# Kernel tuning notes

Hardware: AMD Instinct MI355X
Metric: run time of the kernel (lower is better)

## Reference

```python
import jax, jax.numpy as jnp
import numpy as np

DIM = 1024
HEADS = 16
HEAD_DIM = DIM // HEADS
SCALE = float(HEAD_DIM) ** -0.5


def setup_inputs() -> dict:
    key = jax.random.key(0)
    k1, k2, k3 = jax.random.split(key, 3)
    x = jax.random.normal(k1, (4, 2048, DIM), dtype=jnp.float32)
    w_qkv = jax.random.normal(k2, (DIM, 3 * DIM), dtype=jnp.float32) * (DIM ** -0.5)
    b_qkv = jnp.zeros((3 * DIM,), dtype=jnp.float32)
    w_proj = jax.random.normal(k3, (DIM, DIM), dtype=jnp.float32) * (DIM ** -0.5)
    b_proj = jnp.zeros((DIM,), dtype=jnp.float32)
    return {"x": x, "w_qkv": w_qkv, "b_qkv": b_qkv, "w_proj": w_proj, "b_proj": b_proj}


def reference(x, w_qkv, b_qkv, w_proj, b_proj):
    B, N, D = x.shape
    # QKV projection -> [B, N, 3, H, Dh] -> split
    qkv = (x @ w_qkv + b_qkv).reshape(B, N, 3, HEADS, HEAD_DIM)
    q = qkv[:, :, 0].transpose(0, 2, 1, 3)  # [B, H, N, Dh]
    k = qkv[:, :, 1].transpose(0, 2, 1, 3)
    v = qkv[:, :, 2].transpose(0, 2, 1, 3)
    att = jnp.einsum("bhnd,bhmd->bhnm", q, k) * SCALE  # [B, H, N, N]
    att = jax.nn.softmax(att, axis=-1)
    out = jnp.einsum("bhnm,bhmd->bhnd", att, v)  # [B, H, N, Dh]
    out = out.transpose(0, 2, 1, 3).reshape(B, N, D)
    return out @ w_proj + b_proj
```

## Files before the change

kernel.cpp:

```cpp
#include <hip/hip_runtime.h>


typedef __attribute__((ext_vector_type(8))) short bf8v;
typedef __attribute__((ext_vector_type(4))) short bf4v;
typedef __attribute__((ext_vector_type(4))) float f32x4;

#define DEVINL __device__ __forceinline__

DEVINL unsigned short f2bf(float x){
    unsigned int u = __float_as_uint(x);
    return (unsigned short)((u + 0x7FFFu + ((u >> 16) & 1u)) >> 16);
}
DEVINL float bf2f(unsigned short b){ return __uint_as_float(((unsigned int)b) << 16); }

union BV { bf8v v; unsigned int u[4]; };

DEVINL void gload16(const unsigned short* g, unsigned short* l){
    __builtin_amdgcn_global_load_lds(
        (const __attribute__((address_space(1))) unsigned int*)g,
        (__attribute__((address_space(3))) unsigned int*)l, 16, 0, 0);
}

__global__ __launch_bounds__(256) void split_rm(const float* __restrict__ in,
        unsigned short* __restrict__ oh, int n4){
    int i = blockIdx.x * 256 + threadIdx.x;
    if (i >= n4) return;
    float4 v = reinterpret_cast<const float4*>(in)[i];
    float vv[4] = {v.x, v.y, v.z, v.w};
    bf4v h;
#pragma unroll
    for (int j = 0; j < 4; ++j) h[j] = (short)f2bf(vv[j]);
    *reinterpret_cast<bf4v*>(oh + (size_t)i * 4) = h;
}

__global__ __launch_bounds__(256) void transpose_split(const float* __restrict__ in,
        unsigned short* __restrict__ oh,
        int K, int N){
    __shared__ float tile[32][33];
    int n0 = blockIdx.x * 32, k0 = blockIdx.y * 32;
    int c = threadIdx.x & 31, r0 = threadIdx.x >> 5;
#pragma unroll
    for (int j = 0; j < 4; ++j){
        int r = r0 + j * 8;
        tile[r][c] = in[(size_t)(k0 + r) * N + n0 + c];
    }
    __syncthreads();
#pragma unroll
    for (int j = 0; j < 4; ++j){
        int r = r0 + j * 8;
        float v = tile[c][r];
        oh[(size_t)(n0 + r) * K + k0 + c] = f2bf(v);
    }
}

template<int EPI, int NPL>
__global__ __launch_bounds__(256) void gemm3k(
    const unsigned short* __restrict__ Ah, const unsigned short* __restrict__ Al,
    const unsigned short* __restrict__ Bh,
    const float* __restrict__ bias, float* __restrict__ outf,
    unsigned short* __restrict__ Qh,
    unsigned short* __restrict__ Kh,
    unsigned short* __restrict__ Vth)
{
    __shared__ unsigned short AldsH[3][4096];
    __shared__ unsigned short AldsL[NPL == 2 ? 3 : 1][4096];
    __shared__ unsigned short Blds [3][4096];
    const int t = threadIdx.x;
    const int l = t & 63, g = l >> 4, wv = t >> 6;
    const int wr = wv >> 1, wc = wv & 1;
    const int bm = blockIdx.y * 128, bn = blockIdx.x * 128;
    const int srow = t >> 2;
    const int scol = ((t & 3) ^ ((t >> 3) & 3)) * 8;

    f32x4 acc[4][4] = {};

    auto stage = [&](int kt, int buf){
        int klocal = kt * 32;
#pragma unroll
        for (int j = 0; j < 2; ++j){
            size_t ro = (size_t)(bm + j*64 + srow) * 1024 + klocal + scol;
            gload16(Ah + ro, &AldsH[buf][j*2048 + wv*512]);
            if (NPL == 2) gload16(Al + ro, &AldsL[buf][j*2048 + wv*512]);
            gload16(Bh + (size_t)(bn + j*64 + srow) * 1024 + klocal + scol,
                    &Blds[buf][j*2048 + wv*512]);
        }
    };
    auto compute = [&](int cur){
        bf8v afh[4], bfv[4];
#pragma unroll
        for (int mf = 0; mf < 4; ++mf){
            int ar = wr*64 + mf*16 + (l & 15);
            afh[mf] = *reinterpret_cast<const bf8v*>(
                &AldsH[cur][ar*32 + (g ^ ((ar >> 1) & 3))*8]);
        }
#pragma unroll
        for (int nf = 0; nf < 4; ++nf){
            int br = wc*64 + nf*16 + (l & 15);
            bfv[nf] = *reinterpret_cast<const bf8v*>(
                &Blds[cur][br*32 + (g ^ ((br >> 1) & 3))*8]);
        }
#pragma unroll
        for (int mf = 0; mf < 4; ++mf)
#pragma unroll
            for (int nf = 0; nf < 4; ++nf)
                acc[mf][nf] = __builtin_amdgcn_mfma_f32_16x16x32_bf16(afh[mf], bfv[nf], acc[mf][nf], 0, 0, 0);
        if (NPL == 2){
            bf8v afl[4];
#pragma unroll
            for (int mf = 0; mf < 4; ++mf){
                int ar = wr*64 + mf*16 + (l & 15);
                afl[mf] = *reinterpret_cast<const bf8v*>(
                    &AldsL[NPL == 2 ? cur : 0][ar*32 + (g ^ ((ar >> 1) & 3))*8]);
            }
#pragma unroll
            for (int mf = 0; mf < 4; ++mf)
#pragma unroll
                for (int nf = 0; nf < 4; ++nf)
                    acc[mf][nf] = __builtin_amdgcn_mfma_f32_16x16x32_bf16(afl[mf], bfv[nf], acc[mf][nf], 0, 0, 0);
        }
    };

    stage(0, 0);
    stage(1, 1);
    if constexpr (NPL == 2) asm volatile("s_waitcnt vmcnt(6)" ::: "memory");
    else                    asm volatile("s_waitcnt vmcnt(4)" ::: "memory");
    __builtin_amdgcn_s_barrier();
    __builtin_amdgcn_sched_barrier(0);

    int cur = 0, nxt = 1, nx2 = 2;
#pragma unroll 1
    for (int kt = 0; kt < 32; ++kt){
        if (kt + 2 < 32) stage(kt + 2, nx2);
        compute(cur);
        if (kt + 1 < 32){
            if (kt + 2 < 32){
                if constexpr (NPL == 2) asm volatile("s_waitcnt vmcnt(6)" ::: "memory");
                else                    asm volatile("s_waitcnt vmcnt(4)" ::: "memory");
            } else {
                asm volatile("s_waitcnt vmcnt(0)" ::: "memory");
            }
            __builtin_amdgcn_s_barrier();
            __builtin_amdgcn_sched_barrier(0);
        }
        int tmp = cur; cur = nxt; nxt = nx2; nx2 = tmp;
    }
#pragma unroll
    for (int mf = 0; mf < 4; ++mf)
#pragma unroll
    for (int nf = 0; nf < 4; ++nf)
#pragma unroll
    for (int r = 0; r < 4; ++r){
        int n = bn + wc*64 + nf*16 + (l & 15);
        int m = bm + wr*64 + mf*16 + g*4 + r;
        float v = acc[mf][nf][r] + bias[n];
        if (EPI == 0){
            int sec = n >> 10;
            int nn = n & 1023, hh = nn >> 6, dh = nn & 63;
            int bb = m >> 11, tok = m & 2047;
            if (sec == 0) v *= 0.18033688011112042f;
            unsigned short hb = f2bf(v);
            if (sec == 2){
                int tok2 = (tok & ~31) | (((tok >> 2) & 3) << 3) | (tok & 3) | (((tok >> 4) & 1) << 2);
                tok2 = (tok2 & ~31) | ((tok2 & 31) ^ (((dh >> 1) & 3) << 3));
                size_t o = ((size_t)((bb*16 + hh)*64 + dh)) * 2048 + tok2;
                Vth[o] = hb;
            } else if (sec == 1){
                size_t o = ((size_t)((bb*16 + hh)*2048 + tok)) * 64 + (dh ^ ((tok & 7) << 3));
                Kh[o] = hb;
            } else {
                size_t o = ((size_t)((bb*16 + hh)*2048 + tok)) * 64 + dh;
                Qh[o] = hb;
            }
        } else {
            outf[(size_t)m * 1024 + n] = v;
        }
    }
}

__global__ __launch_bounds__(256, 3) void attn(
    const unsigned short* __restrict__ Qh,
    const unsigned short* __restrict__ Kh,
    const unsigned short* __restrict__ Vth,
    unsigned short* __restrict__ Oh, unsigned short* __restrict__ Ol)
{
    __shared__ unsigned short Klds[2][2048];
    __shared__ unsigned short Vlds[2][2048];
    const int t = threadIdx.x, l = t & 63, g = l >> 4, wv = t >> 6;
    const int bid = (int)((blockIdx.x & 7) * 128 + (blockIdx.x >> 3));
    const int qt = bid & 15, hh = (bid >> 4) & 15, bb = bid >> 8;
    const int bh = bb * 16 + hh;
    const int q0 = qt * 128 + wv * 32;

    const unsigned short* Kbh = Kh  + (size_t)bh * 131072;
    const unsigned short* Vbh = Vth + (size_t)bh * 131072;

    const int kst = (t >> 3) * 64   + (t & 7) * 8;
    const int vst = (t >> 2) * 2048 + (t & 3) * 8;

    bf8v qh_[2][2];
#pragma unroll
    for (int nf = 0; nf < 2; ++nf){
        size_t ro = ((size_t)bh * 2048 + q0 + nf*16 + (l & 15)) * 64 + g * 8;
#pragma unroll
        for (int ks = 0; ks < 2; ++ks)
            qh_[nf][ks] = *reinterpret_cast<const bf8v*>(Qh + ro + ks*32);
    }
    f32x4 ot[4][2] = {};
    float l_run[2] = {0.f, 0.f};

    auto stage = [&](int it, int buf){
        gload16(Kbh + it*2048 + kst, &Klds[buf][wv*512]);
        gload16(Vbh + it*32   + vst, &Vlds[buf][wv*512]);
    };
    auto step = [&](int cur){
        bf8v kf[2][2], vf[4];
#pragma unroll
        for (int mf = 0; mf < 2; ++mf){
            int r = (l & 15) + 16*mf;
#pragma unroll
            for (int ks = 0; ks < 2; ++ks)
                kf[mf][ks] = *reinterpret_cast<const bf8v*>(
                    &Klds[cur][r*64 + ((g*8 + ks*32) ^ ((r & 7) << 3))]);
        }
#pragma unroll
        for (int mf = 0; mf < 4; ++mf){
            int dh = (l & 15) + 16*mf;
            vf[mf] = *reinterpret_cast<const bf8v*>(
                &Vlds[cur][dh*32 + ((g*8) ^ (((dh >> 1) & 3) << 3))]);
        }
        f32x4 s[2][2] = {};
        __builtin_amdgcn_s_setprio(1);
#pragma unroll
        for (int mf = 0; mf < 2; ++mf)
#pragma unroll
        for (int nf = 0; nf < 2; ++nf)
#pragma unroll
        for (int ks = 0; ks < 2; ++ks)
            s[mf][nf] = __builtin_amdgcn_mfma_f32_16x16x32_bf16(kf[mf][ks], qh_[nf][ks], s[mf][nf], 0,0,0);
        __builtin_amdgcn_s_setprio(0);
        BV ph[2];
#pragma unroll
        for (int nf = 0; nf < 2; ++nf){
            float p[8];
#pragma unroll
            for (int mf = 0; mf < 2; ++mf)
#pragma unroll
            for (int r = 0; r < 4; ++r)
                p[mf*4 + r] = __builtin_amdgcn_exp2f(s[mf][nf][r]);
            l_run[nf] += ((p[0]+p[1]) + (p[2]+p[3])) + ((p[4]+p[5]) + (p[6]+p[7]));
#pragma unroll
            for (int i = 0; i < 4; ++i){
                unsigned u0 = __float_as_uint(p[2*i]);
                unsigned u1 = __float_as_uint(p[2*i+1]);
                u0 += 0x7FFFu + ((u0 >> 16) & 1u);
                u1 += 0x7FFFu + ((u1 >> 16) & 1u);
                ph[nf].u[i] = __builtin_amdgcn_perm(u1, u0, 0x07060302u);
            }
        }
        __builtin_amdgcn_s_setprio(1);
#pragma unroll
        for (int mf = 0; mf < 4; ++mf)
#pragma unroll
        for (int nf = 0; nf < 2; ++nf)
            ot[mf][nf] = __builtin_amdgcn_mfma_f32_16x16x32_bf16(vf[mf], ph[nf].v, ot[mf][nf], 0,0,0);
        __builtin_amdgcn_s_setprio(0);
    };

    stage(0, 0);
    __syncthreads();
#pragma unroll 1
    for (int it = 0; it < 64; it += 2){
        stage(it + 1, 1);
        step(0);
        __syncthreads();
        if (it + 2 < 64) stage(it + 2, 0);
        step(1);
        __syncthreads();
    }
#pragma unroll
    for (int nf = 0; nf < 2; ++nf){
        float lr = l_run[nf];
        lr += __shfl_xor(lr, 16);
        lr += __shfl_xor(lr, 32);
        float inv = 1.f / lr;
        int tok = q0 + nf*16 + (l & 15);
#pragma unroll
        for (int mf = 0; mf < 4; ++mf){
            bf4v hv, lv;
#pragma unroll
            for (int r = 0; r < 4; ++r){
                float v = ot[mf][nf][r] * inv;
                unsigned short hb = f2bf(v);
                hv[r] = (short)hb;
                lv[r] = (short)f2bf(v - bf2f(hb));
            }
            size_t o = ((size_t)(bb * 2048 + tok)) * 1024 + hh*64 + mf*16 + g*4;
            *reinterpret_cast<bf4v*>(Oh + o) = hv;
            *reinterpret_cast<bf4v*>(Ol + o) = lv;
        }
    }
}

extern "C" void kernel_launch(void* const* d_in, const int* in_sizes, int n_in,
                              void* d_out, int out_size, void* d_ws, size_t ws_size,
                              hipStream_t stream) {
    (void)in_sizes; (void)n_in; (void)out_size; (void)ws_size;
    const float* x      = (const float*)d_in[0];
    const float* w_qkv  = (const float*)d_in[1];
    const float* b_qkv  = (const float*)d_in[2];
    const float* w_proj = (const float*)d_in[3];
    const float* b_proj = (const float*)d_in[4];
    float* out = (float*)d_out;

    char* w = (char*)d_ws;
    unsigned short* XH  = (unsigned short*)(w + 0);
    unsigned short* ATL = (unsigned short*)(w + 16777216);
    unsigned short* QH  = (unsigned short*)(w + 33554432);
    unsigned short* KH  = (unsigned short*)(w + 67108864);
    unsigned short* VTH = (unsigned short*)(w + 100663296);
    unsigned short* WQH = (unsigned short*)(w + 134217728);
    unsigned short* WPH = (unsigned short*)(w + 140509184);
    unsigned short* ATH = XH;

    split_rm<<<8192, 256, 0, stream>>>(x, XH, 2097152);
    transpose_split<<<dim3(96, 32), 256, 0, stream>>>(w_qkv, WQH, 1024, 3072);
    transpose_split<<<dim3(32, 32), 256, 0, stream>>>(w_proj, WPH, 1024, 1024);
    gemm3k<0,1><<<dim3(24, 64), 256, 0, stream>>>(XH, nullptr, WQH, b_qkv, nullptr,
                                                  QH, KH, VTH);
    attn<<<1024, 256, 0, stream>>>(QH, KH, VTH, ATH, ATL);
    gemm3k<1,2><<<dim3(8, 64), 256, 0, stream>>>(ATH, ATL, WPH, b_proj, out,
                                                 nullptr, nullptr, nullptr);
}
```

Before: 228.3 us.

## Triple-buffer K/V tiles with vmcnt-based waits, pack bf16 via hardware convert

```diff
diff --git a/kernel.cpp b/kernel.cpp
--- a/kernel.cpp
+++ b/kernel.cpp
@@ -177,14 +177,14 @@
     }
 }
 
-__global__ __launch_bounds__(256, 3) void attn(
+__global__ __launch_bounds__(256, 4) void attn(
     const unsigned short* __restrict__ Qh,
     const unsigned short* __restrict__ Kh,
     const unsigned short* __restrict__ Vth,
     unsigned short* __restrict__ Oh, unsigned short* __restrict__ Ol)
 {
-    __shared__ unsigned short Klds[2][2048];
-    __shared__ unsigned short Vlds[2][2048];
+    __shared__ unsigned short Klds[3][2048];
+    __shared__ unsigned short Vlds[3][2048];
     const int t = threadIdx.x, l = t & 63, g = l >> 4, wv = t >> 6;
     const int bid = (int)((blockIdx.x & 7) * 128 + (blockIdx.x >> 3));
     const int qt = bid & 15, hh = (bid >> 4) & 15, bb = bid >> 8;
@@ -249,13 +249,9 @@
                 p[mf*4 + r] = __builtin_amdgcn_exp2f(s[mf][nf][r]);
             l_run[nf] += ((p[0]+p[1]) + (p[2]+p[3])) + ((p[4]+p[5]) + (p[6]+p[7]));
 #pragma unroll
-            for (int i = 0; i < 4; ++i){
-                unsigned u0 = __float_as_uint(p[2*i]);
-                unsigned u1 = __float_as_uint(p[2*i+1]);
-                u0 += 0x7FFFu + ((u0 >> 16) & 1u);
-                u1 += 0x7FFFu + ((u1 >> 16) & 1u);
-                ph[nf].u[i] = __builtin_amdgcn_perm(u1, u0, 0x07060302u);
-            }
+            for (int i = 0; i < 4; ++i)
+                asm("v_cvt_pk_bf16_f32 %0, %1, %2"
+                    : "=v"(ph[nf].u[i]) : "v"(p[2*i]), "v"(p[2*i+1]));
         }
         __builtin_amdgcn_s_setprio(1);
 #pragma unroll
@@ -267,15 +263,23 @@
     };
 
     stage(0, 0);
-    __syncthreads();
+    stage(1, 1);
+    asm volatile("s_waitcnt vmcnt(2)" ::: "memory");
+    __builtin_amdgcn_s_barrier();
+    __builtin_amdgcn_sched_barrier(0);
+
+    int cur = 0, nxt = 1, nx2 = 2;
 #pragma unroll 1
-    for (int it = 0; it < 64; it += 2){
-        stage(it + 1, 1);
-        step(0);
-        __syncthreads();
-        if (it + 2 < 64) stage(it + 2, 0);
-        step(1);
-        __syncthreads();
+    for (int it = 0; it < 64; ++it){
+        if (it + 2 < 64) stage(it + 2, nx2);
+        step(cur);
+        if (it + 1 < 64){
+            if (it + 2 < 64) asm volatile("s_waitcnt vmcnt(2)" ::: "memory");
+            else             asm volatile("s_waitcnt vmcnt(0)" ::: "memory");
+            __builtin_amdgcn_s_barrier();
+            __builtin_amdgcn_sched_barrier(0);
+        }
+        int tmp = cur; cur = nxt; nxt = nx2; nx2 = tmp;
     }
 #pragma unroll
     for (int nf = 0; nf < 2; ++nf){
```

Result: faster. 223.3 us (-2.2%).
